# Optimization experiments

Measured on AMD Instinct MI355X. Metric: run time of the kernel, lower is better.

Reference implementation:

```python
import jax, jax.numpy as jnp
import numpy as np

B, N, DIM, HEADS, DIM_HEAD = 2, 2048, 1024, 16, 64
INNER = HEADS * DIM_HEAD
LN_EPS = 1e-5


def setup_inputs() -> dict:
    key = jax.random.key(0)
    k1, k2, k3 = jax.random.split(key, 3)
    x = jax.random.normal(k1, (B, N, DIM), dtype=jnp.float32)
    ln_w = jnp.ones((DIM,), dtype=jnp.float32)
    ln_b = jnp.zeros((DIM,), dtype=jnp.float32)
    w_qkv = jax.random.normal(k2, (DIM, 3 * INNER), dtype=jnp.float32) * (DIM ** -0.5)
    w_out = jax.random.normal(k3, (INNER, DIM), dtype=jnp.float32) * (INNER ** -0.5)
    return {"x": x, "ln_w": ln_w, "ln_b": ln_b, "w_qkv": w_qkv, "w_out": w_out}


def reference(x, ln_w, ln_b, w_qkv, w_out):
    scale = DIM_HEAD ** -0.5
    # LayerNorm over last dim
    mu = jnp.mean(x, axis=-1, keepdims=True)
    var = jnp.var(x, axis=-1, keepdims=True)
    xn = (x - mu) / jnp.sqrt(var + LN_EPS) * ln_w + ln_b
    # qkv projection, split, reshape to b h n d
    qkv = xn @ w_qkv  # [B, N, 3*INNER]
    q, k, v = jnp.split(qkv, 3, axis=-1)
    def to_heads(t):
        return t.reshape(B, N, HEADS, DIM_HEAD).transpose(0, 2, 1, 3)
    q, k, v = to_heads(q) * scale, to_heads(k), to_heads(v)
    # scores + causal mask (triu with offset 1 masked)
    sim = jnp.einsum('bhid,bhjd->bhij', q, k)  # [B, H, N, N]
    causal_mask = jnp.triu(jnp.ones((N, N), dtype=bool), k=1)
    sim = jnp.where(causal_mask, -jnp.finfo(sim.dtype).max, sim)
    attn = jax.nn.softmax(sim, axis=-1)
    out = jnp.einsum('bhij,bhjd->bhid', attn, v)  # [B, H, N, D]
    out = out.transpose(0, 2, 1, 3).reshape(B, N, INNER)
    return out @ w_out
```

## Files before the change

kernel.cpp:

```cpp
#include <hip/hip_runtime.h>
#include <stdint.h>

#define BATCH 2
#define NSEQ  2048
#define DIMC  1024
#define NHEAD 16
#define DHEAD 64
#define QKVN  3072
#define MROWS 4096

typedef __attribute__((ext_vector_type(8))) unsigned short u16x8;
typedef __attribute__((ext_vector_type(4))) unsigned short u16x4;
typedef __attribute__((ext_vector_type(8))) short          bf16x8;
typedef __attribute__((ext_vector_type(4))) float          f32x4;

#define F32_PROBE 0x3F800000u
#define QSCALE 0.18033688f

__device__ __forceinline__ float b2f(unsigned short u) {
  union { unsigned int i; float f; } c; c.i = ((unsigned int)u) << 16; return c.f;
}
__device__ __forceinline__ unsigned short f2b(float f) {
  unsigned int u = __float_as_uint(f);
  return (unsigned short)((u + 0x7fffu + ((u >> 16) & 1u)) >> 16);
}
__device__ __forceinline__ float fast_exp2(float x) {
  return __builtin_amdgcn_exp2f(x);
}
__device__ __forceinline__ void async16(const unsigned short* g, unsigned short* s) {
  __builtin_amdgcn_global_load_lds(
      (const __attribute__((address_space(1))) unsigned int*)g,
      (__attribute__((address_space(3))) unsigned int*)s, 16, 0, 0);
}

__device__ __forceinline__ void tr_tile(const void* __restrict__ in,
                                        unsigned short* __restrict__ out,
                                        int R, int C, int r0, int c0, bool f32,
                                        int t, unsigned short (*tile)[33],
                                        int scale_below) {
  int tx = t & 31, ty = t >> 5;
  float sc = (c0 < scale_below) ? QSCALE : 1.0f;
  if (f32) {
    #pragma unroll
    for (int i = 0; i < 32; i += 8)
      tile[ty + i][tx] = f2b(((const float*)in)[(size_t)(r0 + ty + i) * C + c0 + tx] * sc);
  } else {
    #pragma unroll
    for (int i = 0; i < 32; i += 8)
      tile[ty + i][tx] = f2b(b2f(((const unsigned short*)in)[(size_t)(r0 + ty + i) * C + c0 + tx]) * sc);
  }
  __syncthreads();
  #pragma unroll
  for (int i = 0; i < 32; i += 8)
    out[(size_t)(c0 + ty + i) * R + r0 + tx] = tile[tx][ty + i];
}

__global__ __launch_bounds__(256) void prep_kernel(const void* __restrict__ x,
                                                   const void* __restrict__ w,
                                                   const void* __restrict__ bb,
                                                   unsigned short* __restrict__ xn,
                                                   const void* __restrict__ w_qkv,
                                                   unsigned short* __restrict__ wqkvT,
                                                   const void* __restrict__ w_out,
                                                   unsigned short* __restrict__ woutT,
                                                   const unsigned int* __restrict__ probe) {
  __shared__ unsigned short tile[32][33];
  __shared__ float red[8];
  bool f32 = (*probe == F32_PROBE);
  int bid = blockIdx.x, t = threadIdx.x;

  if (bid < MROWS) {
    int row = bid;
    float v0, v1, v2, v3, w0, w1, w2, w3, bb0, bb1, bb2, bb3;
    if (f32) {
      const float* xr = (const float*)x + (size_t)row * DIMC;
      float4 xv = *(const float4*)(xr + t * 4);
      v0 = xv.x; v1 = xv.y; v2 = xv.z; v3 = xv.w;
      float4 wv = *(const float4*)((const float*)w + t * 4);
      w0 = wv.x; w1 = wv.y; w2 = wv.z; w3 = wv.w;
      float4 bv = *(const float4*)((const float*)bb + t * 4);
      bb0 = bv.x; bb1 = bv.y; bb2 = bv.z; bb3 = bv.w;
    } else {
      const unsigned short* xr = (const unsigned short*)x + (size_t)row * DIMC;
      u16x4 xv = *(const u16x4*)(xr + t * 4);
      v0 = b2f(xv[0]); v1 = b2f(xv[1]); v2 = b2f(xv[2]); v3 = b2f(xv[3]);
      u16x4 wv = *(const u16x4*)((const unsigned short*)w + t * 4);
      w0 = b2f(wv[0]); w1 = b2f(wv[1]); w2 = b2f(wv[2]); w3 = b2f(wv[3]);
      u16x4 bv = *(const u16x4*)((const unsigned short*)bb + t * 4);
      bb0 = b2f(bv[0]); bb1 = b2f(bv[1]); bb2 = b2f(bv[2]); bb3 = b2f(bv[3]);
    }
    float s = v0 + v1 + v2 + v3;
    float q = v0 * v0 + v1 * v1 + v2 * v2 + v3 * v3;
    #pragma unroll
    for (int off = 1; off < 64; off <<= 1) { s += __shfl_xor(s, off); q += __shfl_xor(q, off); }
    int wv_ = t >> 6;
    if ((t & 63) == 0) { red[wv_] = s; red[4 + wv_] = q; }
    __syncthreads();
    s = red[0] + red[1] + red[2] + red[3];
    q = red[4] + red[5] + red[6] + red[7];
    float mu  = s * (1.0f / DIMC);
    float var = q * (1.0f / DIMC) - mu * mu;
    float rstd = rsqrtf(var + 1e-5f);
    u16x4 o;
    o[0] = f2b((v0 - mu) * rstd * w0 + bb0);
    o[1] = f2b((v1 - mu) * rstd * w1 + bb1);
    o[2] = f2b((v2 - mu) * rstd * w2 + bb2);
    o[3] = f2b((v3 - mu) * rstd * w3 + bb3);
    *(u16x4*)(xn + (size_t)row * DIMC + t * 4) = o;
  } else if (bid < MROWS + 3072) {
    int tid = bid - MROWS;
    tr_tile(w_qkv, wqkvT, DIMC, QKVN, (tid / 96) * 32, (tid % 96) * 32, f32, t, tile, 1024);
  } else {
    int tid = bid - (MROWS + 3072);
    tr_tile(w_out, woutT, DIMC, DIMC, (tid >> 5) * 32, (tid & 31) * 32, f32, t, tile, 0);
  }
}

__global__ __launch_bounds__(256) void transpose_kernel(const void* __restrict__ in,
                                                        unsigned short* __restrict__ out,
                                                        int R, int C,
                                                        const unsigned int* __restrict__ probe) {
  __shared__ unsigned short tile[32][33];
  bool f32 = (*probe == F32_PROBE);
  int t = threadIdx.x;
  tr_tile(in, out, R, C, blockIdx.y * 32, blockIdx.x * 32, f32, t, tile, 0);
}

__device__ __forceinline__ void ldA8(bf16x8 (&dst)[8], const unsigned short* base,
                                     int off, int ch0, int ch1) {
  #pragma unroll
  for (int mi = 0; mi < 4; ++mi) {
    dst[mi * 2 + 0] = *(const bf16x8*)&base[off + mi * 1024 + ch0];
    dst[mi * 2 + 1] = *(const bf16x8*)&base[off + mi * 1024 + ch1];
  }
}
__device__ __forceinline__ void ldB4(bf16x8 (&dst)[4], const unsigned short* base,
                                     int off, int ch0, int ch1) {
  #pragma unroll
  for (int ni = 0; ni < 2; ++ni) {
    dst[ni * 2 + 0] = *(const bf16x8*)&base[off + ni * 1024 + ch0];
    dst[ni * 2 + 1] = *(const bf16x8*)&base[off + ni * 1024 + ch1];
  }
}
__device__ __forceinline__ void mfma16q(f32x4 (&acc)[8][4], const bf16x8 (&a)[8],
                                        const bf16x8 (&b)[4], int R, int C) {
  #pragma unroll
  for (int kh = 0; kh < 2; ++kh)
    #pragma unroll
    for (int mi = 0; mi < 4; ++mi)
      #pragma unroll
      for (int ni = 0; ni < 2; ++ni)
        acc[R * 4 + mi][C * 2 + ni] = __builtin_amdgcn_mfma_f32_16x16x32_bf16(
            a[mi * 2 + kh], b[ni * 2 + kh], acc[R * 4 + mi][C * 2 + ni], 0, 0, 0);
}

#define SB    asm volatile("s_barrier" ::: "memory")
#define WVM4  asm volatile("s_waitcnt vmcnt(4)" ::: "memory")
#define WLG0  asm volatile("s_waitcnt lgkmcnt(0)" ::: "memory")
#define PRIO1 __builtin_amdgcn_s_setprio(1)
#define PRIO0 __builtin_amdgcn_s_setprio(0)
#define STG(gp, g, k0, sb) async16((gp) + (size_t)(g) * 65536 + (k0), (sb) + (g) * 4096 + t8)

__global__ __launch_bounds__(512) void gemm1_8p(const unsigned short* __restrict__ A,
                                                const unsigned short* __restrict__ Bt,
                                                unsigned short* __restrict__ C,
                                                unsigned short* __restrict__ vt_out) {
  __shared__ unsigned short lds[65536];
  unsigned short* A0b = lds;
  unsigned short* B0b = lds + 16384;
  unsigned short* A1b = lds + 32768;
  unsigned short* B1b = lds + 49152;

  int t = threadIdx.x;
  int lane = t & 63, wv = t >> 6;
  int l16 = lane & 15, quad = lane >> 4;
  int wr = wv >> 2, wc = wv & 3;

  int bid = blockIdx.x;
  int swzid = (bid & 7) * 24 + (bid >> 3);
  int bx = swzid / 12, by = swzid % 12;
  int bm = bx * 256, bn = by * 256;

  int rl = t >> 3;
  int sc8 = (((t & 7) ^ (rl & 7)) << 3);
  int t8 = t * 8;
  const unsigned short* Ag = A  + (size_t)(bm + rl) * 1024 + sc8;
  const unsigned short* Bg = Bt + (size_t)(bn + rl) * 1024 + sc8;

  int aoff = (wr * 128 + l16) * 64;
  int boff = (wc * 64 + l16) * 64;
  int ch0 = ((quad ^ (l16 & 7)) << 3);
  int ch1 = (((quad + 4) ^ (l16 & 7)) << 3);

  f32x4 acc[8][4] = {};
  bf16x8 ar0[8], ar1[8], bc0[4], bc1[4];

  STG(Ag, 0, 0, A0b); STG(Ag, 1, 0, A0b); STG(Ag, 2, 0, A0b); STG(Ag, 3, 0, A0b);
  STG(Bg, 0, 0, B0b); STG(Bg, 1, 0, B0b); STG(Bg, 2, 0, B0b); STG(Bg, 3, 0, B0b);
  STG(Ag, 0, 64, A1b); STG(Ag, 1, 64, A1b); STG(Ag, 2, 64, A1b); STG(Ag, 3, 64, A1b);
  WVM4;
  SB;

  for (int i = 0; i < 8; ++i) {
    const int k_b1 = (2 * i + 1) * 64;
    const int k_n0 = ((2 * i + 2) & 15) * 64;
    const int k_n1 = ((2 * i + 3) & 15) * 64;

    ldA8(ar0, A0b, aoff, ch0, ch1);
    ldB4(bc0, B0b, boff, ch0, ch1);
    STG(Bg, 0, k_b1, B1b); STG(Bg, 1, k_b1, B1b);
    SB; WLG0; PRIO1; mfma16q(acc, ar0, bc0, 0, 0); PRIO0; SB;
    ldA8(ar1, A0b, aoff + 4096, ch0, ch1);
    STG(Bg, 2, k_b1, B1b); STG(Bg, 3, k_b1, B1b);
    SB; WLG0; PRIO1; mfma16q(acc, ar1, bc0, 1, 0); PRIO0; SB;
    ldB4(bc1, B0b, boff + 2048, ch0, ch1);
    STG(Ag, 0, k_n0, A0b); STG(Ag, 1, k_n0, A0b);
    SB; WLG0; PRIO1; mfma16q(acc, ar0, bc1, 0, 1); PRIO0; SB;
    STG(Ag, 2, k_n0, A0b); STG(Ag, 3, k_n0, A0b);
    WVM4;
    SB; PRIO1; mfma16q(acc, ar1, bc1, 1, 1); PRIO0; SB;

    ldA8(ar0, A1b, aoff, ch0, ch1);
    ldB4(bc0, B1b, boff, ch0, ch1);
    STG(Bg, 0, k_n0, B0b); STG(Bg, 1, k_n0, B0b);
    SB; WLG0; PRIO1; mfma16q(acc, ar0, bc0, 0, 0); PRIO0; SB;
    ldA8(ar1, A1b, aoff + 4096, ch0, ch1);
    STG(Bg, 2, k_n0, B0b); STG(Bg, 3, k_n0, B0b);
    SB; WLG0; PRIO1; mfma16q(acc, ar1, bc0, 1, 0); PRIO0; SB;
    ldB4(bc1, B1b, boff + 2048, ch0, ch1);
    STG(Ag, 0, k_n1, A1b); STG(Ag, 1, k_n1, A1b);
    SB; WLG0; PRIO1; mfma16q(acc, ar0, bc1, 0, 1); PRIO0; SB;
    STG(Ag, 2, k_n1, A1b); STG(Ag, 3, k_n1, A1b);
    WVM4;
    SB; PRIO1; mfma16q(acc, ar1, bc1, 1, 1); PRIO0; SB;
  }

  bool vblk = (bn >= 2048);
  #pragma unroll
  for (int rf = 0; rf < 8; ++rf)
    #pragma unroll
    for (int cf = 0; cf < 4; ++cf) {
      int gr0 = bm + wr * 128 + rf * 16 + quad * 4;
      int gc  = bn + wc * 64 + cf * 16 + l16;
      if (vblk) {
        int hh = (gc >> 6) & 15;
        int dd = gc & 63;
        int bb2 = gr0 >> 11;
        int n0  = gr0 & 2047;
        u16x4 pk;
        #pragma unroll
        for (int r = 0; r < 4; r++) pk[r] = f2b(acc[rf][cf][r]);
        *(u16x4*)&vt_out[(((size_t)(bb2 * 16 + hh) * 64 + dd) << 11) + n0] = pk;
      } else {
        #pragma unroll
        for (int r = 0; r < 4; r++)
          C[(size_t)(gr0 + r) * QKVN + gc] = f2b(acc[rf][cf][r]);
      }
    }
}

__global__ __launch_bounds__(256) void gemm_bt_n64(const unsigned short* __restrict__ A,
                                                   const unsigned short* __restrict__ Bt,
                                                   void* __restrict__ Cv,
                                                   int M, int N, int K, int lda,
                                                   int detect_out,
                                                   const unsigned int* __restrict__ probe) {
  __shared__ unsigned short As[2][128 * 32];
  __shared__ unsigned short Bs[2][64 * 32];
  int t = threadIdx.x;
  int lane = t & 63, wave = t >> 6;
  int l16 = lane & 15, quad = lane >> 4;
  int wm = (wave & 1) * 64, wn = (wave >> 1) * 32;
  int bm = blockIdx.x * 128, bn = blockIdx.y * 64;

  f32x4 acc[4][2] = {};

  int srow = t >> 2;
  int scol = (t & 3) * 8;
  const unsigned short* Ap = A  + (size_t)(bm + srow) * lda + scol;
  const unsigned short* Bp = Bt + (size_t)(bn + srow) * K + scol;
  int so0 = srow * 32 + scol;
  int so1 = (64 + srow) * 32 + scol;

  async16(Ap, &As[0][so0]);
  async16(Ap + (size_t)64 * lda, &As[0][so1]);
  async16(Bp, &Bs[0][so0]);
  __syncthreads();

  int cur = 0;
  for (int k0 = 0; k0 < K; k0 += 32) {
    if (k0 + 32 < K) {
      async16(Ap + k0 + 32, &As[cur ^ 1][so0]);
      async16(Ap + (size_t)64 * lda + k0 + 32, &As[cur ^ 1][so1]);
      async16(Bp + k0 + 32, &Bs[cur ^ 1][so0]);
    }
    bf16x8 af[4], bfr[2];
    #pragma unroll
    for (int mi = 0; mi < 4; mi++)
      af[mi] = *(const bf16x8*)&As[cur][(wm + mi * 16 + l16) * 32 + quad * 8];
    #pragma unroll
    for (int ni = 0; ni < 2; ni++)
      bfr[ni] = *(const bf16x8*)&Bs[cur][(wn + ni * 16 + l16) * 32 + quad * 8];
    PRIO1;
    #pragma unroll
    for (int mi = 0; mi < 4; mi++)
      #pragma unroll
      for (int ni = 0; ni < 2; ni++)
        acc[mi][ni] = __builtin_amdgcn_mfma_f32_16x16x32_bf16(af[mi], bfr[ni], acc[mi][ni], 0, 0, 0);
    PRIO0;
    __syncthreads();
    cur ^= 1;
  }
  bool f32out = detect_out && (*probe == F32_PROBE);
  #pragma unroll
  for (int mi = 0; mi < 4; mi++)
    #pragma unroll
    for (int ni = 0; ni < 2; ni++)
      #pragma unroll
      for (int r = 0; r < 4; r++) {
        int gr = bm + wm + mi * 16 + quad * 4 + r;
        int gc = bn + wn + ni * 16 + l16;
        if (f32out) ((float*)Cv)[(size_t)gr * N + gc] = acc[mi][ni][r];
        else ((unsigned short*)Cv)[(size_t)gr * N + gc] = f2b(acc[mi][ni][r]);
      }
}

__device__ __forceinline__ int swz(int row, int chunk) {
  return row * 64 + ((chunk ^ (row & 7)) << 3);
}

__global__ __launch_bounds__(256) void attn_v5(unsigned short* __restrict__ qkv,
                                               const unsigned short* __restrict__ vt) {
  __shared__ unsigned short lds[20480];

  int t = threadIdx.x;
  int lane = t & 63, w = t >> 6;
  int l16 = lane & 15, quad = lane >> 4;
  int id = blockIdx.x;
  int xcd = id & 7, jj = id >> 3;
  int bh = xcd + ((jj & 3) << 3);
  int qt = 31 - (jj >> 2);
  int b = bh >> 4, h = bh & 15;
  unsigned short* qbase = qkv + (size_t)(b * NSEQ) * QKVN + h * DHEAD;
  const unsigned short* kbase = qbase + 1024;
  const unsigned short* vtb = vt + (size_t)bh * DHEAD * NSEQ;
  unsigned short* Ps = lds + 16384;

  int sr = t >> 3, sc = t & 7;
  int q0 = qt * 64;

  const unsigned short* qp = qbase + (size_t)(q0 + w * 16 + l16) * QKVN + quad * 8;
  bf16x8 bq0 = *(const bf16x8*)(qp);
  bf16x8 bq1 = *(const bf16x8*)(qp + 32);

  float l_i = 0.f;
  f32x4 o[4] = {};
  u16x8 k0r, k1r, v0r, v1r;

  k0r = *(const u16x8*)(kbase + (size_t)sr * QKVN + sc * 8);
  k1r = *(const u16x8*)(kbase + (size_t)(sr + 32) * QKVN + sc * 8);
  v0r = *(const u16x8*)(vtb + (size_t)sr * NSEQ + sc * 8);
  v1r = *(const u16x8*)(vtb + (size_t)(sr + 32) * NSEQ + sc * 8);
  *(u16x8*)&lds[swz(sr, sc)]             = k0r;
  *(u16x8*)&lds[swz(sr + 32, sc)]        = k1r;
  *(u16x8*)&lds[8192 + swz(sr, sc)]      = v0r;
  *(u16x8*)&lds[8192 + swz(sr + 32, sc)] = v1r;
  __syncthreads();

  for (int jt = 0; jt <= qt; jt++) {
    const unsigned short* Kc = lds + (jt & 1) * 4096;
    const unsigned short* Vc = lds + 8192 + (jt & 1) * 4096;

    if (jt < qt) {
      int j0n = (jt + 1) * 64;
      k0r = *(const u16x8*)(kbase + (size_t)(j0n + sr) * QKVN + sc * 8);
      k1r = *(const u16x8*)(kbase + (size_t)(j0n + sr + 32) * QKVN + sc * 8);
      v0r = *(const u16x8*)(vtb + (size_t)sr * NSEQ + j0n + sc * 8);
      v1r = *(const u16x8*)(vtb + (size_t)(sr + 32) * NSEQ + j0n + sc * 8);
    }

    f32x4 s[4];
    #pragma unroll
    for (int mj = 0; mj < 4; mj++)
      #pragma unroll
      for (int r = 0; r < 4; r++) s[mj][r] = -32.0f;
    PRIO1;
    #pragma unroll
    for (int mj = 0; mj < 4; mj++) {
      bf16x8 ak0 = *(const bf16x8*)&Kc[swz(mj * 16 + l16, quad)];
      s[mj] = __builtin_amdgcn_mfma_f32_16x16x32_bf16(ak0, bq0, s[mj], 0, 0, 0);
      bf16x8 ak1 = *(const bf16x8*)&Kc[swz(mj * 16 + l16, 4 + quad)];
      s[mj] = __builtin_amdgcn_mfma_f32_16x16x32_bf16(ak1, bq1, s[mj], 0, 0, 0);
    }
    PRIO0;

    if (jt == qt) {
      int il = w * 16 + l16;
      #pragma unroll
      for (int mj = 0; mj < 4; mj++)
        #pragma unroll
        for (int r = 0; r < 4; r++)
          if (mj * 16 + quad * 4 + r > il) s[mj][r] = -1e30f;
    }

    #pragma unroll
    for (int mj = 0; mj < 4; mj++) {
      u16x4 pk;
      #pragma unroll
      for (int r = 0; r < 4; r++) {
        float p = fast_exp2(s[mj][r]);
        l_i += p;
        pk[r] = f2b(p);
      }
      int ch = mj * 2 + (quad >> 1);
      *(u16x4*)&Ps[swz(w * 16 + l16, ch) + (quad & 1) * 4] = pk;
    }

    PRIO1;
    #pragma unroll
    for (int ks = 0; ks < 2; ks++) {
      bf16x8 ap = *(const bf16x8*)&Ps[swz(w * 16 + l16, ks * 4 + quad)];
      #pragma unroll
      for (int d = 0; d < 4; d++) {
        bf16x8 bv = *(const bf16x8*)&Vc[swz(d * 16 + l16, ks * 4 + quad)];
        o[d] = __builtin_amdgcn_mfma_f32_16x16x32_bf16(ap, bv, o[d], 0, 0, 0);
      }
    }
    PRIO0;

    if (jt < qt) {
      unsigned short* Kn = lds + ((jt + 1) & 1) * 4096;
      unsigned short* Vn = lds + 8192 + ((jt + 1) & 1) * 4096;
      *(u16x8*)&Kn[swz(sr, sc)]      = k0r;
      *(u16x8*)&Kn[swz(sr + 32, sc)] = k1r;
      *(u16x8*)&Vn[swz(sr, sc)]      = v0r;
      *(u16x8*)&Vn[swz(sr + 32, sc)] = v1r;
      __syncthreads();
    }
  }

  l_i += __shfl_xor(l_i, 16);
  l_i += __shfl_xor(l_i, 32);
  #pragma unroll
  for (int r = 0; r < 4; r++) {
    float lr = __shfl(l_i, (lane & 48) | (quad * 4 + r));
    float inv = 1.0f / lr;
    int row = q0 + w * 16 + quad * 4 + r;
    #pragma unroll
    for (int d = 0; d < 4; d++)
      qbase[(size_t)row * QKVN + d * 16 + l16] = f2b(o[d][r] * inv);
  }
}

extern "C" void kernel_launch(void* const* d_in, const int* in_sizes, int n_in,
                              void* d_out, int out_size, void* d_ws, size_t ws_size,
                              hipStream_t stream) {
  const void* x     = d_in[0];
  const void* ln_w  = d_in[1];
  const void* ln_b  = d_in[2];
  const void* w_qkv = d_in[3];
  const void* w_out = d_in[4];
  const unsigned int* probe = (const unsigned int*)d_in[1];

  unsigned short* wqkvT = (unsigned short*)d_ws;
  unsigned short* qkv   = wqkvT + (size_t)QKVN * DIMC;
  unsigned short* xn    = (unsigned short*)d_out;
  size_t base_e  = (size_t)QKVN * DIMC + (size_t)MROWS * QKVN;
  size_t vt_e    = (size_t)BATCH * NHEAD * DHEAD * NSEQ;
  size_t wout_e  = (size_t)DIMC * DIMC;
  bool fit_vt  = ws_size >= (base_e + vt_e) * 2;
  bool fit_all = ws_size >= (base_e + vt_e + wout_e) * 2;
  unsigned short* vtp   = fit_vt ? qkv + (size_t)MROWS * QKVN
                                 : ((unsigned short*)d_out) + ((size_t)4 * 1024 * 1024);
  unsigned short* woutT = fit_all ? vtp + vt_e : wqkvT;

  int prep_blocks = MROWS + 3072 + (fit_all ? 1024 : 0);
  prep_kernel<<<prep_blocks, 256, 0, stream>>>(x, ln_w, ln_b, xn, w_qkv, wqkvT,
                                               w_out, fit_all ? woutT : nullptr, probe);
  gemm1_8p<<<dim3(192), 512, 0, stream>>>(xn, wqkvT, qkv, vtp);
  if (!fit_all)
    transpose_kernel<<<dim3(DIMC / 32, DIMC / 32), 256, 0, stream>>>(w_out, woutT, DIMC, DIMC, probe);
  attn_v5<<<dim3(1024), 256, 0, stream>>>(qkv, vtp);
  gemm_bt_n64<<<dim3(MROWS / 128, DIMC / 64), 256, 0, stream>>>(
      qkv, woutT, d_out, MROWS, DIMC, DIMC, QKVN, 1, probe);
}
```

Before: 180.3 us.

## Split attention KV loop across two wave groups per block with LDS reduction

The attention kernel now runs 512 threads per block, with two groups of four waves each handling alternate 64-key tiles for the same 64-query tile. Each group keeps its own K/V/P buffers in LDS, and the partial outputs and row sums are combined through LDS at the end. Query-tile ordering is also changed so that heavy and light causal tiles are interleaved across block indices. The aim is to halve the serial KV loop length per block and improve load balance. The cost is extra syncs per iteration, larger LDS use, and a final reduction step.

```diff
diff --git a/kernel.cpp b/kernel.cpp
--- a/kernel.cpp
+++ b/kernel.cpp
@@ -329,27 +329,34 @@
   return row * 64 + ((chunk ^ (row & 7)) << 3);
 }
 
-__global__ __launch_bounds__(256) void attn_v5(unsigned short* __restrict__ qkv,
-                                               const unsigned short* __restrict__ vt) {
-  __shared__ unsigned short lds[20480];
+__global__ __launch_bounds__(512, 6) void attn_v6(unsigned short* __restrict__ qkv,
+                                                  const unsigned short* __restrict__ vt) {
+  __shared__ unsigned short lds[24576];
 
   int t = threadIdx.x;
   int lane = t & 63, w = t >> 6;
+  int wg = w & 3, g = w >> 2;
   int l16 = lane & 15, quad = lane >> 4;
+
   int id = blockIdx.x;
   int xcd = id & 7, jj = id >> 3;
   int bh = xcd + ((jj & 3) << 3);
-  int qt = 31 - (jj >> 2);
+  int kk = jj >> 2;
+  int qt = (kk < 16) ? (31 - kk) : (kk - 16);
   int b = bh >> 4, h = bh & 15;
   unsigned short* qbase = qkv + (size_t)(b * NSEQ) * QKVN + h * DHEAD;
   const unsigned short* kbase = qbase + 1024;
   const unsigned short* vtb = vt + (size_t)bh * DHEAD * NSEQ;
-  unsigned short* Ps = lds + 16384;
-
-  int sr = t >> 3, sc = t & 7;
+
+  unsigned short* Kg = lds + g * 4096;
+  unsigned short* Vg = lds + 8192 + g * 4096;
+  unsigned short* Ps = lds + 16384 + g * 4096;
+
+  int tg = t & 255;
+  int sr = tg >> 3, sc = tg & 7;
   int q0 = qt * 64;
 
-  const unsigned short* qp = qbase + (size_t)(q0 + w * 16 + l16) * QKVN + quad * 8;
+  const unsigned short* qp = qbase + (size_t)(q0 + wg * 16 + l16) * QKVN + quad * 8;
   bf16x8 bq0 = *(const bf16x8*)(qp);
   bf16x8 bq1 = *(const bf16x8*)(qp + 32);
 
@@ -357,98 +364,124 @@
   f32x4 o[4] = {};
   u16x8 k0r, k1r, v0r, v1r;
 
-  k0r = *(const u16x8*)(kbase + (size_t)sr * QKVN + sc * 8);
-  k1r = *(const u16x8*)(kbase + (size_t)(sr + 32) * QKVN + sc * 8);
-  v0r = *(const u16x8*)(vtb + (size_t)sr * NSEQ + sc * 8);
-  v1r = *(const u16x8*)(vtb + (size_t)(sr + 32) * NSEQ + sc * 8);
-  *(u16x8*)&lds[swz(sr, sc)]             = k0r;
-  *(u16x8*)&lds[swz(sr + 32, sc)]        = k1r;
-  *(u16x8*)&lds[8192 + swz(sr, sc)]      = v0r;
-  *(u16x8*)&lds[8192 + swz(sr + 32, sc)] = v1r;
+  if (g <= qt) {
+    int j0 = g * 64;
+    k0r = *(const u16x8*)(kbase + (size_t)(j0 + sr) * QKVN + sc * 8);
+    k1r = *(const u16x8*)(kbase + (size_t)(j0 + sr + 32) * QKVN + sc * 8);
+    v0r = *(const u16x8*)(vtb + (size_t)sr * NSEQ + j0 + sc * 8);
+    v1r = *(const u16x8*)(vtb + (size_t)(sr + 32) * NSEQ + j0 + sc * 8);
+    *(u16x8*)&Kg[swz(sr, sc)]      = k0r;
+    *(u16x8*)&Kg[swz(sr + 32, sc)] = k1r;
+    *(u16x8*)&Vg[swz(sr, sc)]      = v0r;
+    *(u16x8*)&Vg[swz(sr + 32, sc)] = v1r;
+  }
   __syncthreads();
 
-  for (int jt = 0; jt <= qt; jt++) {
-    const unsigned short* Kc = lds + (jt & 1) * 4096;
-    const unsigned short* Vc = lds + 8192 + (jt & 1) * 4096;
-
-    if (jt < qt) {
-      int j0n = (jt + 1) * 64;
+  int nits = (qt >> 1) + 1;
+  for (int it = 0; it < nits; ++it) {
+    int jt = 2 * it + g;
+    bool active = (jt <= qt);
+    bool pf = (jt + 2 <= qt);
+
+    if (pf) {
+      int j0n = (jt + 2) * 64;
       k0r = *(const u16x8*)(kbase + (size_t)(j0n + sr) * QKVN + sc * 8);
       k1r = *(const u16x8*)(kbase + (size_t)(j0n + sr + 32) * QKVN + sc * 8);
       v0r = *(const u16x8*)(vtb + (size_t)sr * NSEQ + j0n + sc * 8);
       v1r = *(const u16x8*)(vtb + (size_t)(sr + 32) * NSEQ + j0n + sc * 8);
     }
 
-    f32x4 s[4];
-    #pragma unroll
-    for (int mj = 0; mj < 4; mj++)
-      #pragma unroll
-      for (int r = 0; r < 4; r++) s[mj][r] = -32.0f;
-    PRIO1;
-    #pragma unroll
-    for (int mj = 0; mj < 4; mj++) {
-      bf16x8 ak0 = *(const bf16x8*)&Kc[swz(mj * 16 + l16, quad)];
-      s[mj] = __builtin_amdgcn_mfma_f32_16x16x32_bf16(ak0, bq0, s[mj], 0, 0, 0);
-      bf16x8 ak1 = *(const bf16x8*)&Kc[swz(mj * 16 + l16, 4 + quad)];
-      s[mj] = __builtin_amdgcn_mfma_f32_16x16x32_bf16(ak1, bq1, s[mj], 0, 0, 0);
-    }
-    PRIO0;
-
-    if (jt == qt) {
-      int il = w * 16 + l16;
+    if (active) {
+      f32x4 s[4];
       #pragma unroll
       for (int mj = 0; mj < 4; mj++)
         #pragma unroll
-        for (int r = 0; r < 4; r++)
-          if (mj * 16 + quad * 4 + r > il) s[mj][r] = -1e30f;
-    }
-
-    #pragma unroll
-    for (int mj = 0; mj < 4; mj++) {
-      u16x4 pk;
-      #pragma unroll
-      for (int r = 0; r < 4; r++) {
-        float p = fast_exp2(s[mj][r]);
-        l_i += p;
-        pk[r] = f2b(p);
+        for (int r = 0; r < 4; r++) s[mj][r] = -32.0f;
+      PRIO1;
+      #pragma unroll
+      for (int mj = 0; mj < 4; mj++) {
+        bf16x8 ak0 = *(const bf16x8*)&Kg[swz(mj * 16 + l16, quad)];
+        s[mj] = __builtin_amdgcn_mfma_f32_16x16x32_bf16(ak0, bq0, s[mj], 0, 0, 0);
+        bf16x8 ak1 = *(const bf16x8*)&Kg[swz(mj * 16 + l16, 4 + quad)];
+        s[mj] = __builtin_amdgcn_mfma_f32_16x16x32_bf16(ak1, bq1, s[mj], 0, 0, 0);
       }
-      int ch = mj * 2 + (quad >> 1);
-      *(u16x4*)&Ps[swz(w * 16 + l16, ch) + (quad & 1) * 4] = pk;
-    }
-
-    PRIO1;
-    #pragma unroll
-    for (int ks = 0; ks < 2; ks++) {
-      bf16x8 ap = *(const bf16x8*)&Ps[swz(w * 16 + l16, ks * 4 + quad)];
-      #pragma unroll
-      for (int d = 0; d < 4; d++) {
-        bf16x8 bv = *(const bf16x8*)&Vc[swz(d * 16 + l16, ks * 4 + quad)];
-        o[d] = __builtin_amdgcn_mfma_f32_16x16x32_bf16(ap, bv, o[d], 0, 0, 0);
+      PRIO0;
+
+      if (jt == qt) {
+        int il = wg * 16 + l16;
+        #pragma unroll
+        for (int mj = 0; mj < 4; mj++)
+          #pragma unroll
+          for (int r = 0; r < 4; r++)
+            if (mj * 16 + quad * 4 + r > il) s[mj][r] = -1e30f;
       }
-    }
-    PRIO0;
-
-    if (jt < qt) {
-      unsigned short* Kn = lds + ((jt + 1) & 1) * 4096;
-      unsigned short* Vn = lds + 8192 + ((jt + 1) & 1) * 4096;
-      *(u16x8*)&Kn[swz(sr, sc)]      = k0r;
-      *(u16x8*)&Kn[swz(sr + 32, sc)] = k1r;
-      *(u16x8*)&Vn[swz(sr, sc)]      = v0r;
-      *(u16x8*)&Vn[swz(sr + 32, sc)] = v1r;
-      __syncthreads();
-    }
-  }
-
-  l_i += __shfl_xor(l_i, 16);
-  l_i += __shfl_xor(l_i, 32);
-  #pragma unroll
-  for (int r = 0; r < 4; r++) {
-    float lr = __shfl(l_i, (lane & 48) | (quad * 4 + r));
-    float inv = 1.0f / lr;
-    int row = q0 + w * 16 + quad * 4 + r;
+
+      #pragma unroll
+      for (int mj = 0; mj < 4; mj++) {
+        u16x4 pk;
+        #pragma unroll
+        for (int r = 0; r < 4; r++) {
+          float p = fast_exp2(s[mj][r]);
+          l_i += p;
+          pk[r] = f2b(p);
+        }
+        int ch = mj * 2 + (quad >> 1);
+        *(u16x4*)&Ps[swz(wg * 16 + l16, ch) + (quad & 1) * 4] = pk;
+      }
+
+      PRIO1;
+      #pragma unroll
+      for (int ks = 0; ks < 2; ks++) {
+        bf16x8 ap = *(const bf16x8*)&Ps[swz(wg * 16 + l16, ks * 4 + quad)];
+        #pragma unroll
+        for (int d = 0; d < 4; d++) {
+          bf16x8 bv = *(const bf16x8*)&Vg[swz(d * 16 + l16, ks * 4 + quad)];
+          o[d] = __builtin_amdgcn_mfma_f32_16x16x32_bf16(ap, bv, o[d], 0, 0, 0);
+        }
+      }
+      PRIO0;
+    }
+
+    __syncthreads();
+    if (pf) {
+      *(u16x8*)&Kg[swz(sr, sc)]      = k0r;
+      *(u16x8*)&Kg[swz(sr + 32, sc)] = k1r;
+      *(u16x8*)&Vg[swz(sr, sc)]      = v0r;
+      *(u16x8*)&Vg[swz(sr + 32, sc)] = v1r;
+    }
+    __syncthreads();
+  }
+
+  float* Of = (float*)lds;
+  float* Lf = (float*)lds + 64 * 65;
+  if (g == 1) {
     #pragma unroll
     for (int d = 0; d < 4; d++)
-      qbase[(size_t)row * QKVN + d * 16 + l16] = f2b(o[d][r] * inv);
+      #pragma unroll
+      for (int r = 0; r < 4; r++)
+        Of[(wg * 16 + quad * 4 + r) * 65 + d * 16 + l16] = o[d][r];
+    Lf[wg * 64 + lane] = l_i;
+  }
+  __syncthreads();
+  if (g == 0) {
+    #pragma unroll
+    for (int d = 0; d < 4; d++)
+      #pragma unroll
+      for (int r = 0; r < 4; r++)
+        o[d][r] += Of[(wg * 16 + quad * 4 + r) * 65 + d * 16 + l16];
+    l_i += Lf[wg * 64 + lane];
+
+    l_i += __shfl_xor(l_i, 16);
+    l_i += __shfl_xor(l_i, 32);
+    #pragma unroll
+    for (int r = 0; r < 4; r++) {
+      float lr = __shfl(l_i, (lane & 48) | (quad * 4 + r));
+      float inv = 1.0f / lr;
+      int row = q0 + wg * 16 + quad * 4 + r;
+      #pragma unroll
+      for (int d = 0; d < 4; d++)
+        qbase[(size_t)row * QKVN + d * 16 + l16] = f2b(o[d][r] * inv);
+    }
   }
 }
 
@@ -480,7 +513,7 @@
   gemm1_8p<<<dim3(192), 512, 0, stream>>>(xn, wqkvT, qkv, vtp);
   if (!fit_all)
     transpose_kernel<<<dim3(DIMC / 32, DIMC / 32), 256, 0, stream>>>(w_out, woutT, DIMC, DIMC, probe);
-  attn_v5<<<dim3(1024), 256, 0, stream>>>(qkv, vtp);
+  attn_v6<<<dim3(1024), 512, 0, stream>>>(qkv, vtp);
   gemm_bt_n64<<<dim3(MROWS / 128, DIMC / 64), 256, 0, stream>>>(
       qkv, woutT, d_out, MROWS, DIMC, DIMC, QKVN, 1, probe);
 }
```

After: 183.0 us. About the same (+1.5%).

## Split attention waves over key rows and keep probabilities in registers

Applied to the files above, without the earlier changes.

The attention kernel now assigns each wave a 16-key slice of every 64-key tile instead of a 16-query slice, with all four query blocks held per wave. Probabilities stay in registers and feed 16x16x16 bf16 MFMAs directly, which removes the P round-trip through LDS. K/V tiles are loaded with async global-to-LDS copies, and partial outputs and row sums are reduced across waves through LDS at the end. In exchange the kernel uses more accumulator registers, adds an epilogue reduction with several barriers, and uses inline asm for bf16 packing.

```diff
diff --git a/kernel.cpp b/kernel.cpp
--- a/kernel.cpp
+++ b/kernel.cpp
@@ -12,6 +12,7 @@
 typedef __attribute__((ext_vector_type(8))) unsigned short u16x8;
 typedef __attribute__((ext_vector_type(4))) unsigned short u16x4;
 typedef __attribute__((ext_vector_type(8))) short          bf16x8;
+typedef __attribute__((ext_vector_type(4))) short          s16x4;
 typedef __attribute__((ext_vector_type(4))) float          f32x4;
 
 #define F32_PROBE 0x3F800000u
@@ -31,6 +32,14 @@
   __builtin_amdgcn_global_load_lds(
       (const __attribute__((address_space(1))) unsigned int*)g,
       (__attribute__((address_space(3))) unsigned int*)s, 16, 0, 0);
+}
+__device__ __forceinline__ f32x4 mfma_k16(s16x4 a, s16x4 b, f32x4 c) {
+#if __has_builtin(__builtin_amdgcn_mfma_f32_16x16x16bf16_1k)
+  return __builtin_amdgcn_mfma_f32_16x16x16bf16_1k(a, b, c, 0, 0, 0);
+#else
+  asm("v_mfma_f32_16x16x16_bf16 %0, %1, %2, %0" : "+v"(c) : "v"(a), "v"(b));
+  return c;
+#endif
 }
 
 __device__ __forceinline__ void tr_tile(const void* __restrict__ in,
@@ -328,10 +337,11 @@
 __device__ __forceinline__ int swz(int row, int chunk) {
   return row * 64 + ((chunk ^ (row & 7)) << 3);
 }
-
-__global__ __launch_bounds__(256) void attn_v5(unsigned short* __restrict__ qkv,
-                                               const unsigned short* __restrict__ vt) {
-  __shared__ unsigned short lds[20480];
+#define OSW(d, c) ((d) * 64 + ((((c)) ^ ((d) & 15)) << 2))
+
+__global__ __launch_bounds__(256, 3) void attn_v7(unsigned short* __restrict__ qkv,
+                                                  const unsigned short* __restrict__ vt) {
+  __shared__ unsigned short lds[16384];
 
   int t = threadIdx.x;
   int lane = t & 63, w = t >> 6;
@@ -344,27 +354,26 @@
   unsigned short* qbase = qkv + (size_t)(b * NSEQ) * QKVN + h * DHEAD;
   const unsigned short* kbase = qbase + 1024;
   const unsigned short* vtb = vt + (size_t)bh * DHEAD * NSEQ;
-  unsigned short* Ps = lds + 16384;
 
   int sr = t >> 3, sc = t & 7;
+  int sw8 = ((sc ^ (sr & 7)) << 3);
   int q0 = qt * 64;
 
-  const unsigned short* qp = qbase + (size_t)(q0 + w * 16 + l16) * QKVN + quad * 8;
-  bf16x8 bq0 = *(const bf16x8*)(qp);
-  bf16x8 bq1 = *(const bf16x8*)(qp + 32);
-
-  float l_i = 0.f;
-  f32x4 o[4] = {};
-  u16x8 k0r, k1r, v0r, v1r;
-
-  k0r = *(const u16x8*)(kbase + (size_t)sr * QKVN + sc * 8);
-  k1r = *(const u16x8*)(kbase + (size_t)(sr + 32) * QKVN + sc * 8);
-  v0r = *(const u16x8*)(vtb + (size_t)sr * NSEQ + sc * 8);
-  v1r = *(const u16x8*)(vtb + (size_t)(sr + 32) * NSEQ + sc * 8);
-  *(u16x8*)&lds[swz(sr, sc)]             = k0r;
-  *(u16x8*)&lds[swz(sr + 32, sc)]        = k1r;
-  *(u16x8*)&lds[8192 + swz(sr, sc)]      = v0r;
-  *(u16x8*)&lds[8192 + swz(sr + 32, sc)] = v1r;
+  bf16x8 bq0[4], bq1[4];
+  #pragma unroll
+  for (int qb = 0; qb < 4; qb++) {
+    const unsigned short* qp = qbase + (size_t)(q0 + qb * 16 + l16) * QKVN + quad * 8;
+    bq0[qb] = *(const bf16x8*)(qp);
+    bq1[qb] = *(const bf16x8*)(qp + 32);
+  }
+
+  float l4[4] = {0.f, 0.f, 0.f, 0.f};
+  f32x4 o[4][4] = {};
+
+  async16(kbase + (size_t)sr * QKVN + sw8,              lds + t * 8);
+  async16(kbase + (size_t)(sr + 32) * QKVN + sw8,       lds + 2048 + t * 8);
+  async16(vtb + (size_t)sr * NSEQ + sw8,                lds + 8192 + t * 8);
+  async16(vtb + (size_t)(sr + 32) * NSEQ + sw8,         lds + 8192 + 2048 + t * 8);
   __syncthreads();
 
   for (int jt = 0; jt <= qt; jt++) {
@@ -373,82 +382,124 @@
 
     if (jt < qt) {
       int j0n = (jt + 1) * 64;
-      k0r = *(const u16x8*)(kbase + (size_t)(j0n + sr) * QKVN + sc * 8);
-      k1r = *(const u16x8*)(kbase + (size_t)(j0n + sr + 32) * QKVN + sc * 8);
-      v0r = *(const u16x8*)(vtb + (size_t)sr * NSEQ + j0n + sc * 8);
-      v1r = *(const u16x8*)(vtb + (size_t)(sr + 32) * NSEQ + j0n + sc * 8);
-    }
-
-    f32x4 s[4];
-    #pragma unroll
-    for (int mj = 0; mj < 4; mj++)
-      #pragma unroll
-      for (int r = 0; r < 4; r++) s[mj][r] = -32.0f;
-    PRIO1;
-    #pragma unroll
-    for (int mj = 0; mj < 4; mj++) {
-      bf16x8 ak0 = *(const bf16x8*)&Kc[swz(mj * 16 + l16, quad)];
-      s[mj] = __builtin_amdgcn_mfma_f32_16x16x32_bf16(ak0, bq0, s[mj], 0, 0, 0);
-      bf16x8 ak1 = *(const bf16x8*)&Kc[swz(mj * 16 + l16, 4 + quad)];
-      s[mj] = __builtin_amdgcn_mfma_f32_16x16x32_bf16(ak1, bq1, s[mj], 0, 0, 0);
-    }
-    PRIO0;
-
-    if (jt == qt) {
-      int il = w * 16 + l16;
-      #pragma unroll
-      for (int mj = 0; mj < 4; mj++)
-        #pragma unroll
-        for (int r = 0; r < 4; r++)
-          if (mj * 16 + quad * 4 + r > il) s[mj][r] = -1e30f;
-    }
-
-    #pragma unroll
-    for (int mj = 0; mj < 4; mj++) {
-      u16x4 pk;
-      #pragma unroll
-      for (int r = 0; r < 4; r++) {
-        float p = fast_exp2(s[mj][r]);
-        l_i += p;
-        pk[r] = f2b(p);
-      }
-      int ch = mj * 2 + (quad >> 1);
-      *(u16x4*)&Ps[swz(w * 16 + l16, ch) + (quad & 1) * 4] = pk;
-    }
-
-    PRIO1;
-    #pragma unroll
-    for (int ks = 0; ks < 2; ks++) {
-      bf16x8 ap = *(const bf16x8*)&Ps[swz(w * 16 + l16, ks * 4 + quad)];
-      #pragma unroll
-      for (int d = 0; d < 4; d++) {
-        bf16x8 bv = *(const bf16x8*)&Vc[swz(d * 16 + l16, ks * 4 + quad)];
-        o[d] = __builtin_amdgcn_mfma_f32_16x16x32_bf16(ap, bv, o[d], 0, 0, 0);
-      }
-    }
-    PRIO0;
-
-    if (jt < qt) {
       unsigned short* Kn = lds + ((jt + 1) & 1) * 4096;
       unsigned short* Vn = lds + 8192 + ((jt + 1) & 1) * 4096;
-      *(u16x8*)&Kn[swz(sr, sc)]      = k0r;
-      *(u16x8*)&Kn[swz(sr + 32, sc)] = k1r;
-      *(u16x8*)&Vn[swz(sr, sc)]      = v0r;
-      *(u16x8*)&Vn[swz(sr + 32, sc)] = v1r;
-      __syncthreads();
-    }
-  }
-
-  l_i += __shfl_xor(l_i, 16);
-  l_i += __shfl_xor(l_i, 32);
-  #pragma unroll
-  for (int r = 0; r < 4; r++) {
-    float lr = __shfl(l_i, (lane & 48) | (quad * 4 + r));
-    float inv = 1.0f / lr;
-    int row = q0 + w * 16 + quad * 4 + r;
-    #pragma unroll
-    for (int d = 0; d < 4; d++)
-      qbase[(size_t)row * QKVN + d * 16 + l16] = f2b(o[d][r] * inv);
+      async16(kbase + (size_t)(j0n + sr) * QKVN + sw8,      Kn + t * 8);
+      async16(kbase + (size_t)(j0n + sr + 32) * QKVN + sw8, Kn + 2048 + t * 8);
+      async16(vtb + (size_t)sr * NSEQ + j0n + sw8,          Vn + t * 8);
+      async16(vtb + (size_t)(sr + 32) * NSEQ + j0n + sw8,   Vn + 2048 + t * 8);
+    }
+
+    bf16x8 ak0 = *(const bf16x8*)&Kc[swz(w * 16 + l16, quad)];
+    bf16x8 ak1 = *(const bf16x8*)&Kc[swz(w * 16 + l16, 4 + quad)];
+    f32x4 sv[4];
+    PRIO1;
+    #pragma unroll
+    for (int qb = 0; qb < 4; qb++) {
+      f32x4 s = {-32.0f, -32.0f, -32.0f, -32.0f};
+      s = __builtin_amdgcn_mfma_f32_16x16x32_bf16(ak0, bq0[qb], s, 0, 0, 0);
+      s = __builtin_amdgcn_mfma_f32_16x16x32_bf16(ak1, bq1[qb], s, 0, 0, 0);
+      sv[qb] = s;
+    }
+    PRIO0;
+
+    s16x4 pa[4];
+    #pragma unroll
+    for (int qb = 0; qb < 4; qb++) {
+      float p0 = fast_exp2(sv[qb][0]);
+      float p1 = fast_exp2(sv[qb][1]);
+      float p2 = fast_exp2(sv[qb][2]);
+      float p3 = fast_exp2(sv[qb][3]);
+      if (jt == qt) {
+        int jl = w * 16 + quad * 4, ql = qb * 16 + l16;
+        if (jl + 0 > ql) p0 = 0.f;
+        if (jl + 1 > ql) p1 = 0.f;
+        if (jl + 2 > ql) p2 = 0.f;
+        if (jl + 3 > ql) p3 = 0.f;
+      }
+      l4[qb] += (p0 + p1) + (p2 + p3);
+      union { unsigned int u[2]; s16x4 v; } cc;
+      asm("v_cvt_pk_bf16_f32 %0, %1, %2" : "=v"(cc.u[0]) : "v"(p0), "v"(p1));
+      asm("v_cvt_pk_bf16_f32 %0, %1, %2" : "=v"(cc.u[1]) : "v"(p2), "v"(p3));
+      pa[qb] = cc.v;
+    }
+
+    PRIO1;
+    #pragma unroll
+    for (int db = 0; db < 4; db++) {
+      u16x4 vb = *(const u16x4*)&Vc[swz(db * 16 + l16, 2 * w + (quad >> 1)) + (quad & 1) * 4];
+      union { u16x4 u; s16x4 s; } vc; vc.u = vb;
+      #pragma unroll
+      for (int qb = 0; qb < 4; qb++)
+        o[qb][db] = mfma_k16(pa[qb], vc.s, o[qb][db]);
+    }
+    PRIO0;
+
+    if (jt < qt) __syncthreads();
+  }
+
+  #pragma unroll
+  for (int qb = 0; qb < 4; qb++) {
+    l4[qb] += __shfl_xor(l4[qb], 16);
+    l4[qb] += __shfl_xor(l4[qb], 32);
+  }
+  __syncthreads();
+  float* f = (float*)lds;
+  if (quad == 0) {
+    #pragma unroll
+    for (int qb = 0; qb < 4; qb++) f[w * 64 + qb * 16 + l16] = l4[qb];
+  }
+  __syncthreads();
+  #pragma unroll
+  for (int qb = 0; qb < 4; qb++)
+    l4[qb] = (f[qb * 16 + l16] + f[64 + qb * 16 + l16]) +
+             (f[128 + qb * 16 + l16] + f[192 + qb * 16 + l16]);
+  __syncthreads();
+
+  float* r0 = f;
+  float* r1 = f + 4096;
+  if (w == 1 || w == 3) {
+    float* rg = (w == 1) ? r0 : r1;
+    #pragma unroll
+    for (int qb = 0; qb < 4; qb++)
+      #pragma unroll
+      for (int db = 0; db < 4; db++)
+        *(f32x4*)&rg[OSW(db * 16 + l16, qb * 4 + quad)] = o[qb][db];
+  }
+  __syncthreads();
+  if (w == 0 || w == 2) {
+    float* rg = (w == 0) ? r0 : r1;
+    #pragma unroll
+    for (int qb = 0; qb < 4; qb++)
+      #pragma unroll
+      for (int db = 0; db < 4; db++)
+        o[qb][db] += *(const f32x4*)&rg[OSW(db * 16 + l16, qb * 4 + quad)];
+  }
+  __syncthreads();
+  if (w == 2) {
+    #pragma unroll
+    for (int qb = 0; qb < 4; qb++)
+      #pragma unroll
+      for (int db = 0; db < 4; db++)
+        *(f32x4*)&r0[OSW(db * 16 + l16, qb * 4 + quad)] = o[qb][db];
+  }
+  __syncthreads();
+  if (w == 0) {
+    #pragma unroll
+    for (int qb = 0; qb < 4; qb++) {
+      #pragma unroll
+      for (int db = 0; db < 4; db++)
+        o[qb][db] += *(const f32x4*)&r0[OSW(db * 16 + l16, qb * 4 + quad)];
+      #pragma unroll
+      for (int r = 0; r < 4; r++) {
+        float lr = __shfl(l4[qb], (lane & 48) | (quad * 4 + r));
+        float inv = 1.0f / lr;
+        int row = q0 + qb * 16 + quad * 4 + r;
+        #pragma unroll
+        for (int db = 0; db < 4; db++)
+          qbase[(size_t)row * QKVN + db * 16 + l16] = f2b(o[qb][db][r] * inv);
+      }
+    }
   }
 }
 
@@ -480,7 +531,7 @@
   gemm1_8p<<<dim3(192), 512, 0, stream>>>(xn, wqkvT, qkv, vtp);
   if (!fit_all)
     transpose_kernel<<<dim3(DIMC / 32, DIMC / 32), 256, 0, stream>>>(w_out, woutT, DIMC, DIMC, probe);
-  attn_v5<<<dim3(1024), 256, 0, stream>>>(qkv, vtp);
+  attn_v7<<<dim3(1024), 256, 0, stream>>>(qkv, vtp);
   gemm_bt_n64<<<dim3(MROWS / 128, DIMC / 64), 256, 0, stream>>>(
       qkv, woutT, d_out, MROWS, DIMC, DIMC, QKVN, 1, probe);
 }
```

Result: faster. 174.8 us (-3.1%).
